# Kernel optimization log

Hardware: AMD Instinct MI355X
Metric: run time of the kernel (lower is better)

The kernel has to match this reference:

```python
import jax, jax.numpy as jnp
import numpy as np

IMAGE_C = 1
IMAGE_W = 28
PIXELS_PER_ROW = IMAGE_W * IMAGE_C  # 28

B, T, E = 16, IMAGE_W * IMAGE_W * IMAGE_C, 512  # T = 784
H = 8
D = E // H  # head_dim = 64


def get_2d_causal_bias(T):
    idx = jnp.arange(T)
    i = idx // PIXELS_PER_ROW          # row index
    j = (idx % PIXELS_PER_ROW) // IMAGE_C  # col index
    c = idx % IMAGE_C                  # channel index
    q_i, k_i = i[:, None], i[None, :]
    q_j, k_j = j[:, None], j[None, :]
    q_c, k_c = c[:, None], c[None, :]
    allowed = (k_i < q_i) | ((k_i == q_i) & (k_j < q_j)) | (
        (k_i == q_i) & (k_j == q_j) & (k_c <= q_c))
    bias = jnp.where(allowed, 0.0, -jnp.inf).astype(jnp.float32)
    return bias[None, None]  # [1, 1, T, T]


def setup_inputs() -> dict:
    key = jax.random.key(0)
    ks = jax.random.split(key, 5)
    s = 1.0 / np.sqrt(E)
    return {
        "x": jax.random.normal(ks[0], (B, T, E), dtype=jnp.float32),
        "Wq": jax.random.normal(ks[1], (E, E), dtype=jnp.float32) * s,
        "bq": jnp.zeros((E,), dtype=jnp.float32),
        "Wk": jax.random.normal(ks[2], (E, E), dtype=jnp.float32) * s,
        "bk": jnp.zeros((E,), dtype=jnp.float32),
        "Wv": jax.random.normal(ks[3], (E, E), dtype=jnp.float32) * s,
        "bv": jnp.zeros((E,), dtype=jnp.float32),
        "Wo": jax.random.normal(ks[4], (E, E), dtype=jnp.float32) * s,
        "bo": jnp.zeros((E,), dtype=jnp.float32),
    }


def reference(x, Wq, bq, Wk, bk, Wv, bv, Wo, bo):
    Bx, Tx, Ex = x.shape
    # projections (torch Linear: y = x @ W.T + b; here W stored as [E, E] used directly)
    Q = (x @ Wq + bq).reshape(Bx, Tx, H, D).transpose(0, 2, 1, 3)  # [B,H,T,D]
    K = (x @ Wk + bk).reshape(Bx, Tx, H, D).transpose(0, 2, 1, 3)
    V = (x @ Wv + bv).reshape(Bx, Tx, H, D).transpose(0, 2, 1, 3)
    scores = jnp.einsum("bhqd,bhkd->bhqk", Q, K) / jnp.sqrt(jnp.float32(D))
    scores = scores + get_2d_causal_bias(Tx)
    attn = jax.nn.softmax(scores, axis=-1)
    ctx = jnp.einsum("bhqk,bhkd->bhqd", attn, V)
    ctx = ctx.transpose(0, 2, 1, 3).reshape(Bx, Tx, Ex)
    return ctx @ Wo + bo
```

## Files before the change

kernel.cpp:

```cpp
#include <hip/hip_runtime.h>
#include <hip/hip_bf16.h>

#define BB    16
#define TT    784
#define TPK   832
#define TPQ   896
#define EE    512
#define HH    8
#define DD    64
#define BT    (BB*TT)

typedef short short8 __attribute__((ext_vector_type(8)));
typedef short short4v __attribute__((ext_vector_type(4)));
typedef float floatx4 __attribute__((ext_vector_type(4)));
typedef float floatx16 __attribute__((ext_vector_type(16)));
typedef unsigned uint4v __attribute__((ext_vector_type(4)));

__device__ __forceinline__ short f2bf(float f) {
    unsigned u = __builtin_bit_cast(unsigned, f);
    u += 0x7FFFu + ((u >> 16) & 1u);
    return (short)(u >> 16);
}

__device__ __forceinline__ unsigned cvtpk_bf16(float lo, float hi) {
    unsigned r;
    asm("v_cvt_pk_bf16_f32 %0, %1, %2" : "=v"(r) : "v"(lo), "v"(hi));
    return r;
}

__device__ __forceinline__ void gload_lds16(const short* g, short* l) {
    __builtin_amdgcn_global_load_lds(
        (const __attribute__((address_space(1))) void*)g,
        (__attribute__((address_space(3))) void*)l, 16, 0, 0);
}

__global__ void prep_kernel(const float* __restrict__ x, short* __restrict__ xb,
                            const float* __restrict__ Wq, const float* __restrict__ Wk,
                            const float* __restrict__ Wv, short* __restrict__ wqkvt,
                            const float* __restrict__ Wo, short* __restrict__ wot,
                            short* __restrict__ Qb, short* __restrict__ Kb, short* __restrict__ Vt)
{
    __shared__ short t[64][65];
    int b = blockIdx.x;
    if (b < 3136) {
        int i = (b * 256 + threadIdx.x) * 8;
        float4 a = *(const float4*)(x + i);
        float4 c = *(const float4*)(x + i + 4);
        short8 o;
        o[0] = f2bf(a.x); o[1] = f2bf(a.y); o[2] = f2bf(a.z); o[3] = f2bf(a.w);
        o[4] = f2bf(c.x); o[5] = f2bf(c.y); o[6] = f2bf(c.z); o[7] = f2bf(c.w);
        *(short8*)(xb + i) = o;
    } else if (b < 3392) {
        const float* W; short* out; int n0, k0;
        if (b < 3328) {
            int tt = b - 3136;
            n0 = (tt % 24) * 64; k0 = (tt / 24) * 64;
            W = (n0 < 512) ? Wq : (n0 < 1024 ? Wk : Wv);
            out = wqkvt;
        } else {
            int tt = b - 3328;
            n0 = (tt % 8) * 64; k0 = (tt / 8) * 64;
            W = Wo; out = wot;
        }
        int nn0 = n0 & 511;
        for (int i = threadIdx.x; i < 4096; i += 256) {
            int r = i >> 6, c = i & 63;
            t[r][c] = f2bf(W[(k0 + r) * 512 + nn0 + c]);
        }
        __syncthreads();
        for (int i = threadIdx.x; i < 4096; i += 256) {
            int nr = i >> 6, kc = i & 63;
            out[(n0 + nr) * 512 + k0 + kc] = t[kc][nr];
        }
    } else {
        int c = (b - 3392) * 256 + threadIdx.x;
        short8 z = (short8){0,0,0,0,0,0,0,0};
        if (c < 114688) {
            int bh = c / 896, j = c - bh * 896;
            *(short8*)&Qb[(bh * TPQ + TT) * 64 + j * 8] = z;
        } else if (c < 163840) {
            int c2 = c - 114688;
            int bh = c2 / 384, j = c2 - bh * 384;
            *(short8*)&Kb[(bh * TPK + TT) * 64 + j * 8] = z;
        } else {
            int c3 = c - 163840;
            int bh = c3 / 384, j = c3 - bh * 384;
            int d = j / 6, m = j - d * 6;
            *(short8*)&Vt[(bh * 64 + d) * TPK + TT + m * 8] = z;
        }
    }
}

__global__ __launch_bounds__(256, 3) void gemm_qkv_kernel(
    const short* __restrict__ A, const short* __restrict__ Bt,
    const float* __restrict__ bq, const float* __restrict__ bk, const float* __restrict__ bv,
    short* __restrict__ Qb, short* __restrict__ Kb, short* __restrict__ Vt)
{
    __shared__ __align__(16) short smem[24576];
    short* As0 = smem;
    short* Bs0 = smem + 12288;

    const int orig = blockIdx.x;
    const int tile = (orig & 7) * 147 + (orig >> 3);
    const int m0 = (tile / 12) * 128, n0 = (tile % 12) * 128;
    const int tid = threadIdx.x;
    const int lane = tid & 63, w = tid >> 6;
    const int wr = w >> 1, wc = w & 1;
    const int l16 = lane & 15, quad = lane >> 4;

    const int sr = tid & 127;
    const int sc = tid >> 7;
    const short* Ag = A  + (size_t)(m0 + sr) * 512 + sc * 8;
    const short* Bg = Bt + (size_t)(n0 + sr) * 512 + sc * 8;

    auto stage = [&](int it) {
        int b = it % 3;
        int ko = it * 32;
        gload_lds16(Ag + ko,      As0 + b * 4096 + tid * 8);
        gload_lds16(Ag + ko + 16, As0 + b * 4096 + 2048 + tid * 8);
        gload_lds16(Bg + ko,      Bs0 + b * 4096 + tid * 8);
        gload_lds16(Bg + ko + 16, Bs0 + b * 4096 + 2048 + tid * 8);
    };

    floatx4 acc[4][4];
    #pragma unroll
    for (int i = 0; i < 4; i++)
        #pragma unroll
        for (int j = 0; j < 4; j++)
            acc[i][j] = (floatx4){0.f, 0.f, 0.f, 0.f};

    stage(0);
    stage(1);

    #pragma unroll
    for (int it = 0; it < 16; it++) {
        if (it < 15) asm volatile("s_waitcnt vmcnt(4)" ::: "memory");
        else         asm volatile("s_waitcnt vmcnt(0)" ::: "memory");
        __builtin_amdgcn_s_barrier();
        __builtin_amdgcn_sched_barrier(0);
        if (it < 14) stage(it + 2);
        const short* as = As0 + (it % 3) * 4096;
        const short* bs = Bs0 + (it % 3) * 4096;
        short8 af[4], bf[4];
        #pragma unroll
        for (int i = 0; i < 4; i++) {
            af[i] = *(const short8*)&as[quad * 1024 + (wr * 64 + i * 16 + l16) * 8];
            bf[i] = *(const short8*)&bs[quad * 1024 + (wc * 64 + i * 16 + l16) * 8];
        }
        #pragma unroll
        for (int mi = 0; mi < 4; mi++)
            #pragma unroll
            for (int ni = 0; ni < 4; ni++)
                acc[mi][ni] = __builtin_amdgcn_mfma_f32_16x16x32_bf16(af[mi], bf[ni], acc[mi][ni], 0, 0, 0);
    }
    __syncthreads();

    const int sel = n0 >> 9;
    if (sel == 2) {
        #pragma unroll
        for (int mi = 0; mi < 4; mi++) {
            int m = m0 + wr * 64 + mi * 16 + quad * 4;
            int bb = m / TT, t = m - bb * TT;
            #pragma unroll
            for (int ni = 0; ni < 4; ni++) {
                int nn = (n0 + wc * 64 + ni * 16 + l16) & 511;
                int hh = nn >> 6, dd = nn & 63;
                float b = bv[nn];
                short4v pv;
                #pragma unroll
                for (int r = 0; r < 4; r++) pv[r] = f2bf(acc[mi][ni][r] + b);
                *(short4v*)&Vt[((size_t)(bb * HH + hh) * 64 + dd) * TPK + t] = pv;
            }
        }
    } else {
        short* Ct = smem;
        const float* bias = (sel == 0) ? bq : bk;
        #pragma unroll
        for (int mi = 0; mi < 4; mi++) {
            #pragma unroll
            for (int ni = 0; ni < 4; ni++) {
                int nl = wc * 64 + ni * 16 + l16;
                int nn = (n0 + nl) & 511;
                float b = bias[nn];
                #pragma unroll
                for (int r = 0; r < 4; r++) {
                    float v = acc[mi][ni][r] + b;
                    if (sel == 0) v *= 0.125f;
                    Ct[(wr * 64 + mi * 16 + quad * 4 + r) * 130 + nl] = f2bf(v);
                }
            }
        }
        __syncthreads();
        short* dst = (sel == 0) ? Qb : Kb;
        const int tp = (sel == 0) ? TPQ : TPK;
        int nl = lane * 2;
        int nn = (n0 + nl) & 511;
        int hh = nn >> 6, dd = nn & 63;
        #pragma unroll 4
        for (int rr = 0; rr < 32; rr++) {
            int ml = w * 32 + rr;
            int m = m0 + ml;
            int bb = m / TT, t = m - bb * TT;
            unsigned pv = *(const unsigned*)&Ct[ml * 130 + nl];
            *(unsigned*)&dst[((bb * HH + hh) * tp + t) * 64 + dd] = pv;
        }
    }
}

__global__ __launch_bounds__(256, 3) void attn_kernel(
    const short* __restrict__ Qb, const short* __restrict__ Kb, const short* __restrict__ Vt,
    short* __restrict__ ctx)
{
    const int g = blockIdx.x;
    const int low = g & 7, rest = g >> 3;
    const int qt = 12 - (rest >> 4);
    const int bh = ((rest & 15) << 3) | low;
    const int bb = bh >> 3, hh = bh & 7;
    const int tid = threadIdx.x;
    const int lane = tid & 63, w = tid >> 6;
    const int wq = w >> 1, wk = w & 1;
    const int l32 = lane & 31, hi = lane >> 5;
    const int r7 = l32 & 7;

    __shared__ __align__(16) short Ks[2][4096];
    __shared__ __align__(16) short Vs[2][4096];

    const short* Kbase = Kb + (size_t)(bh * TPK) * 64;
    const short* Vbase = Vt + (size_t)(bh * 64) * TPK;

    const int srow = tid >> 3;
    const int sc8  = tid & 7;
    const int scol = sc8 * 8;
    const int ksw  = (sc8 ^ (srow & 7)) * 8;
    const int vg0  = (sc8 >> 1) * 2;
    const int vsw0 = ((vg0       ^ (srow & 7)) * 8) + (sc8 & 1) * 4;
    const int vsw1 = (((vg0 + 1) ^ (srow & 7)) * 8) + (sc8 & 1) * 4;

    short8 kreg[2], vreg[2];
    auto load_tile = [&](int kt) {
        #pragma unroll
        for (int p = 0; p < 2; p++) {
            int row = srow + p * 32;
            kreg[p] = *(const short8*)(Kbase + (kt * 64 + row) * 64 + scol);
            vreg[p] = *(const short8*)(Vbase + row * TPK + kt * 64 + scol);
        }
    };
    auto store_tile = [&](int b) {
        #pragma unroll
        for (int p = 0; p < 2; p++) {
            int ro = (srow + p * 32) * 64;
            *(short8*)&Ks[b][ro + ksw] = kreg[p];
            short4v v0, v1;
            #pragma unroll
            for (int i = 0; i < 4; i++) { v0[i] = vreg[p][i]; v1[i] = vreg[p][i + 4]; }
            *(short4v*)&Vs[b][ro + vsw0] = v0;
            *(short4v*)&Vs[b][ro + vsw1] = v1;
        }
    };

    const int q_lo = qt * 64 + wq * 32;
    const int qg = q_lo + l32;
    const bool wreal = (q_lo < TT);
    const short* Qrow = Qb + (size_t)(bh * TPQ + qg) * 64;
    short8 qf[4];
    #pragma unroll
    for (int d = 0; d < 4; d++) qf[d] = *(const short8*)(Qrow + d * 16 + hi * 8);

    floatx16 accO[2];
    #pragma unroll
    for (int dt = 0; dt < 2; dt++)
        #pragma unroll
        for (int i = 0; i < 16; i++) accO[dt][i] = 0.f;
    float accL = 0.f;

    load_tile(0);
    store_tile(0);

    for (int kt = 0; kt <= qt; kt++) {
        const int cb = kt & 1;
        if (kt < qt) load_tile(kt + 1);
        __syncthreads();
        const int kbase = kt * 64 + wk * 32;
        if (wreal && kbase <= q_lo + 31) {
            floatx16 z;
            #pragma unroll
            for (int i = 0; i < 16; i++) z[i] = 0.f;
            #pragma unroll
            for (int d = 0; d < 4; d++) {
                short8 kf = *(const short8*)&Ks[cb][(wk * 32 + l32) * 64 + (((d * 2 + hi) ^ r7) * 8)];
                z = __builtin_amdgcn_mfma_f32_32x32x16_bf16(kf, qf[d], z, 0, 0, 0);
            }
            float p[16];
            #pragma unroll
            for (int r = 0; r < 16; r++) p[r] = __expf(z[r]);
            if (kbase + 31 > q_lo) {
                #pragma unroll
                for (int r = 0; r < 16; r++) {
                    int keyg = kbase + (r & 3) + 8 * (r >> 2) + 4 * hi;
                    if (keyg > qg) p[r] = 0.f;
                }
            }
            #pragma unroll
            for (int r = 0; r < 16; r++) accL += p[r];
            #pragma unroll
            for (int s = 0; s < 2; s++) {
                uint4v pw;
                #pragma unroll
                for (int jj = 0; jj < 4; jj++)
                    pw[jj] = cvtpk_bf16(p[8 * s + 2 * jj], p[8 * s + 2 * jj + 1]);
                short8 pb = __builtin_bit_cast(short8, pw);
                #pragma unroll
                for (int dt = 0; dt < 2; dt++) {
                    short8 vf = *(const short8*)&Vs[cb][(dt * 32 + l32) * 64 + (((wk * 4 + s * 2 + hi) ^ r7) * 8)];
                    accO[dt] = __builtin_amdgcn_mfma_f32_32x32x16_bf16(vf, pb, accO[dt], 0, 0, 0);
                }
            }
        }
        if (kt < qt) store_tile((kt + 1) & 1);
    }

    __syncthreads();
    float* rbuf  = (float*)&Ks[0][0];
    float* rbufL = (float*)&Vs[0][0];
    if (wk == 1) {
        #pragma unroll
        for (int dt = 0; dt < 2; dt++)
            #pragma unroll
            for (int r = 0; r < 16; r++)
                rbuf[((wq * 2 + dt) * 16 + r) * 64 + lane] = accO[dt][r];
        rbufL[wq * 64 + lane] = accL;
    }
    __syncthreads();
    if (wk == 0) {
        #pragma unroll
        for (int dt = 0; dt < 2; dt++)
            #pragma unroll
            for (int r = 0; r < 16; r++)
                accO[dt][r] += rbuf[((wq * 2 + dt) * 16 + r) * 64 + lane];
        accL += rbufL[wq * 64 + lane];
        float Lt = accL + __shfl_xor(accL, 32, 64);
        if (wreal && qg < TT) {
            float inv = 1.f / Lt;
            short* crow = ctx + (size_t)(bb * TT + qg) * 512 + hh * 64;
            #pragma unroll
            for (int dt = 0; dt < 2; dt++)
                #pragma unroll
                for (int g4 = 0; g4 < 4; g4++) {
                    short4v pv;
                    #pragma unroll
                    for (int r4 = 0; r4 < 4; r4++) pv[r4] = f2bf(accO[dt][g4 * 4 + r4] * inv);
                    *(short4v*)&crow[dt * 32 + g4 * 8 + 4 * hi] = pv;
                }
        }
    }
}

__global__ __launch_bounds__(256, 4) void gemm_out_kernel(
    const short* __restrict__ A, const short* __restrict__ Bt,
    const float* __restrict__ bo, float* __restrict__ out)
{
    __shared__ __align__(16) short smem[16384];
    short* As0 = smem;
    short* Bs0 = smem + 8192;

    const int orig = blockIdx.x;
    const int tile = (orig & 7) * 49 + (orig >> 3);
    const int m0 = (tile >> 2) * 128, n0 = (tile & 3) * 128;
    const int tid = threadIdx.x;
    const int lane = tid & 63, w = tid >> 6;
    const int wr = w >> 1, wc = w & 1;
    const int l16 = lane & 15, quad = lane >> 4;

    const int srow = w * 32 + (lane >> 2);
    const int scol = (lane & 3) * 8;
    const short* Ag = A  + (size_t)(m0 + srow) * 512 + scol;
    const short* Bg = Bt + (size_t)(n0 + srow) * 512 + scol;
    short* Abase = As0 + w * 1024;
    short* Bbase = Bs0 + w * 1024;

    auto stage = [&](int it) {
        int b = it & 1;
        int ko = it * 32;
        gload_lds16(Ag + ko,            Abase + b * 4096);
        gload_lds16(Ag + ko + 16 * 512, Abase + b * 4096 + 512);
        gload_lds16(Bg + ko,            Bbase + b * 4096);
        gload_lds16(Bg + ko + 16 * 512, Bbase + b * 4096 + 512);
    };

    floatx4 acc[4][4];
    #pragma unroll
    for (int i = 0; i < 4; i++)
        #pragma unroll
        for (int j = 0; j < 4; j++)
            acc[i][j] = (floatx4){0.f, 0.f, 0.f, 0.f};

    stage(0);
    __syncthreads();

    for (int it = 0; it < 16; it++) {
        if (it < 15) stage(it + 1);
        const short* as = As0 + (it & 1) * 4096;
        const short* bs = Bs0 + (it & 1) * 4096;
        short8 af[4], bf[4];
        #pragma unroll
        for (int i = 0; i < 4; i++) {
            af[i] = *(const short8*)&as[(wr * 64 + i * 16 + l16) * 32 + quad * 8];
            bf[i] = *(const short8*)&bs[(wc * 64 + i * 16 + l16) * 32 + quad * 8];
        }
        #pragma unroll
        for (int mi = 0; mi < 4; mi++)
            #pragma unroll
            for (int ni = 0; ni < 4; ni++)
                acc[mi][ni] = __builtin_amdgcn_mfma_f32_16x16x32_bf16(af[mi], bf[ni], acc[mi][ni], 0, 0, 0);
        __syncthreads();
    }

    #pragma unroll
    for (int mi = 0; mi < 4; mi++) {
        #pragma unroll
        for (int ni = 0; ni < 4; ni++) {
            int n = n0 + wc * 64 + ni * 16 + l16;
            float bias = bo[n];
            #pragma unroll
            for (int r = 0; r < 4; r++) {
                int m = m0 + wr * 64 + mi * 16 + quad * 4 + r;
                out[(size_t)m * 512 + n] = acc[mi][ni][r] + bias;
            }
        }
    }
}

extern "C" void kernel_launch(void* const* d_in, const int* in_sizes, int n_in,
                              void* d_out, int out_size, void* d_ws, size_t ws_size,
                              hipStream_t stream) {
    const float* x  = (const float*)d_in[0];
    const float* Wq = (const float*)d_in[1];
    const float* bq = (const float*)d_in[2];
    const float* Wk = (const float*)d_in[3];
    const float* bk = (const float*)d_in[4];
    const float* Wv = (const float*)d_in[5];
    const float* bv = (const float*)d_in[6];
    const float* Wo = (const float*)d_in[7];
    const float* bo = (const float*)d_in[8];
    float* out = (float*)d_out;

    char* ws = (char*)d_ws;
    size_t off = 0;
    auto alloc = [&](size_t bytes) -> void* {
        void* p = ws + off;
        off += (bytes + 255) & ~(size_t)255;
        return p;
    };
    short* xb    = (short*)alloc((size_t)BT * EE * 2);
    short* wqkvt = (short*)alloc((size_t)1536 * 512 * 2);
    short* wot   = (short*)alloc((size_t)512 * 512 * 2);
    short* Qb    = (short*)alloc((size_t)BB * HH * TPQ * DD * 2);
    short* Kb    = (short*)alloc((size_t)BB * HH * TPK * DD * 2);
    short* Vtb   = (short*)alloc((size_t)BB * HH * DD * TPK * 2);
    short* ctxb  = (short*)alloc((size_t)BT * EE * 2);

    prep_kernel<<<4224, 256, 0, stream>>>(x, xb, Wq, Wk, Wv, wqkvt, Wo, wot, Qb, Kb, Vtb);
    gemm_qkv_kernel<<<1176, 256, 0, stream>>>(xb, wqkvt, bq, bk, bv, Qb, Kb, Vtb);
    attn_kernel<<<1664, 256, 0, stream>>>(Qb, Kb, Vtb, ctxb);
    gemm_out_kernel<<<392, 256, 0, stream>>>(ctxb, wot, bo, out);
}
```

Baseline: 174.4 us.

## Give each attention wave its own query rows; triple-buffer output GEMM

The attention kernel now gives each of the four waves its own 32 query rows over a 128-query block and has each wave process both 32-key halves of a tile. This removes the cross-wave LDS reduction and halves the grid, so each K/V tile staged in LDS is shared by more queries. The output GEMM moves to a three-stage async LDS pipeline with explicit vmcnt waits and a single barrier per iteration, plus a k-major LDS layout. The price is lower occupancy in the GEMM (launch bound 3, more LDS), coarser causal work imbalance, and more serial work per attention wave.

```diff
diff --git a/kernel.cpp b/kernel.cpp
--- a/kernel.cpp
+++ b/kernel.cpp
@@ -213,12 +213,11 @@
 {
     const int g = blockIdx.x;
     const int low = g & 7, rest = g >> 3;
-    const int qt = 12 - (rest >> 4);
+    const int qb = 6 - (rest >> 4);
     const int bh = ((rest & 15) << 3) | low;
     const int bb = bh >> 3, hh = bh & 7;
     const int tid = threadIdx.x;
     const int lane = tid & 63, w = tid >> 6;
-    const int wq = w >> 1, wk = w & 1;
     const int l32 = lane & 31, hi = lane >> 5;
     const int r7 = l32 & 7;
 
@@ -258,9 +257,13 @@
         }
     };
 
-    const int q_lo = qt * 64 + wq * 32;
-    const int qg = q_lo + l32;
+    const int q0   = qb * 128;
+    const int q_lo = q0 + w * 32;
+    const int qg   = q_lo + l32;
     const bool wreal = (q_lo < TT);
+    const int q_top = (q0 + 127 < TT - 1) ? (q0 + 127) : (TT - 1);
+    const int KT = (q_top >> 6) + 1;
+
     const short* Qrow = Qb + (size_t)(bh * TPQ + qg) * 64;
     short8 qf[4];
     #pragma unroll
@@ -276,92 +279,76 @@
     load_tile(0);
     store_tile(0);
 
-    for (int kt = 0; kt <= qt; kt++) {
+    for (int kt = 0; kt < KT; kt++) {
         const int cb = kt & 1;
-        if (kt < qt) load_tile(kt + 1);
+        if (kt < KT - 1) load_tile(kt + 1);
         __syncthreads();
-        const int kbase = kt * 64 + wk * 32;
-        if (wreal && kbase <= q_lo + 31) {
-            floatx16 z;
-            #pragma unroll
-            for (int i = 0; i < 16; i++) z[i] = 0.f;
-            #pragma unroll
-            for (int d = 0; d < 4; d++) {
-                short8 kf = *(const short8*)&Ks[cb][(wk * 32 + l32) * 64 + (((d * 2 + hi) ^ r7) * 8)];
-                z = __builtin_amdgcn_mfma_f32_32x32x16_bf16(kf, qf[d], z, 0, 0, 0);
-            }
-            float p[16];
-            #pragma unroll
-            for (int r = 0; r < 16; r++) p[r] = __expf(z[r]);
-            if (kbase + 31 > q_lo) {
-                #pragma unroll
-                for (int r = 0; r < 16; r++) {
-                    int keyg = kbase + (r & 3) + 8 * (r >> 2) + 4 * hi;
-                    if (keyg > qg) p[r] = 0.f;
+        if (wreal) {
+            #pragma unroll
+            for (int kh = 0; kh < 2; kh++) {
+                const int kbase = kt * 64 + kh * 32;
+                if (kbase > q_lo + 31) continue;
+                floatx16 z;
+                #pragma unroll
+                for (int i = 0; i < 16; i++) z[i] = 0.f;
+                #pragma unroll
+                for (int d = 0; d < 4; d++) {
+                    short8 kf = *(const short8*)&Ks[cb][(kh * 32 + l32) * 64 + (((d * 2 + hi) ^ r7) * 8)];
+                    z = __builtin_amdgcn_mfma_f32_32x32x16_bf16(kf, qf[d], z, 0, 0, 0);
+                }
+                float p[16];
+                #pragma unroll
+                for (int r = 0; r < 16; r++) p[r] = __expf(z[r]);
+                if (kbase + 31 > q_lo) {
+                    #pragma unroll
+                    for (int r = 0; r < 16; r++) {
+                        int keyg = kbase + (r & 3) + 8 * (r >> 2) + 4 * hi;
+                        if (keyg > qg) p[r] = 0.f;
+                    }
+                }
+                #pragma unroll
+                for (int r = 0; r < 16; r++) accL += p[r];
+                #pragma unroll
+                for (int s = 0; s < 2; s++) {
+                    uint4v pw;
+                    #pragma unroll
+                    for (int jj = 0; jj < 4; jj++)
+                        pw[jj] = cvtpk_bf16(p[8 * s + 2 * jj], p[8 * s + 2 * jj + 1]);
+                    short8 pb = __builtin_bit_cast(short8, pw);
+                    #pragma unroll
+                    for (int dt = 0; dt < 2; dt++) {
+                        short8 vf = *(const short8*)&Vs[cb][(dt * 32 + l32) * 64 + (((kh * 4 + s * 2 + hi) ^ r7) * 8)];
+                        accO[dt] = __builtin_amdgcn_mfma_f32_32x32x16_bf16(vf, pb, accO[dt], 0, 0, 0);
+                    }
                 }
             }
-            #pragma unroll
-            for (int r = 0; r < 16; r++) accL += p[r];
-            #pragma unroll
-            for (int s = 0; s < 2; s++) {
-                uint4v pw;
-                #pragma unroll
-                for (int jj = 0; jj < 4; jj++)
-                    pw[jj] = cvtpk_bf16(p[8 * s + 2 * jj], p[8 * s + 2 * jj + 1]);
-                short8 pb = __builtin_bit_cast(short8, pw);
-                #pragma unroll
-                for (int dt = 0; dt < 2; dt++) {
-                    short8 vf = *(const short8*)&Vs[cb][(dt * 32 + l32) * 64 + (((wk * 4 + s * 2 + hi) ^ r7) * 8)];
-                    accO[dt] = __builtin_amdgcn_mfma_f32_32x32x16_bf16(vf, pb, accO[dt], 0, 0, 0);
-                }
+        }
+        if (kt < KT - 1) store_tile((kt + 1) & 1);
+    }
+
+    float Lt = accL + __shfl_xor(accL, 32, 64);
+    if (wreal && qg < TT) {
+        float inv = 1.f / Lt;
+        short* crow = ctx + (size_t)(bb * TT + qg) * 512 + hh * 64;
+        #pragma unroll
+        for (int dt = 0; dt < 2; dt++)
+            #pragma unroll
+            for (int g4 = 0; g4 < 4; g4++) {
+                short4v pv;
+                #pragma unroll
+                for (int r4 = 0; r4 < 4; r4++) pv[r4] = f2bf(accO[dt][g4 * 4 + r4] * inv);
+                *(short4v*)&crow[dt * 32 + g4 * 8 + 4 * hi] = pv;
             }
-        }
-        if (kt < qt) store_tile((kt + 1) & 1);
-    }
-
-    __syncthreads();
-    float* rbuf  = (float*)&Ks[0][0];
-    float* rbufL = (float*)&Vs[0][0];
-    if (wk == 1) {
-        #pragma unroll
-        for (int dt = 0; dt < 2; dt++)
-            #pragma unroll
-            for (int r = 0; r < 16; r++)
-                rbuf[((wq * 2 + dt) * 16 + r) * 64 + lane] = accO[dt][r];
-        rbufL[wq * 64 + lane] = accL;
-    }
-    __syncthreads();
-    if (wk == 0) {
-        #pragma unroll
-        for (int dt = 0; dt < 2; dt++)
-            #pragma unroll
-            for (int r = 0; r < 16; r++)
-                accO[dt][r] += rbuf[((wq * 2 + dt) * 16 + r) * 64 + lane];
-        accL += rbufL[wq * 64 + lane];
-        float Lt = accL + __shfl_xor(accL, 32, 64);
-        if (wreal && qg < TT) {
-            float inv = 1.f / Lt;
-            short* crow = ctx + (size_t)(bb * TT + qg) * 512 + hh * 64;
-            #pragma unroll
-            for (int dt = 0; dt < 2; dt++)
-                #pragma unroll
-                for (int g4 = 0; g4 < 4; g4++) {
-                    short4v pv;
-                    #pragma unroll
-                    for (int r4 = 0; r4 < 4; r4++) pv[r4] = f2bf(accO[dt][g4 * 4 + r4] * inv);
-                    *(short4v*)&crow[dt * 32 + g4 * 8 + 4 * hi] = pv;
-                }
-        }
-    }
-}
-
-__global__ __launch_bounds__(256, 4) void gemm_out_kernel(
+    }
+}
+
+__global__ __launch_bounds__(256, 3) void gemm_out_kernel(
     const short* __restrict__ A, const short* __restrict__ Bt,
     const float* __restrict__ bo, float* __restrict__ out)
 {
-    __shared__ __align__(16) short smem[16384];
+    __shared__ __align__(16) short smem[24576];
     short* As0 = smem;
-    short* Bs0 = smem + 8192;
+    short* Bs0 = smem + 12288;
 
     const int orig = blockIdx.x;
     const int tile = (orig & 7) * 49 + (orig >> 3);
@@ -371,20 +358,18 @@
     const int wr = w >> 1, wc = w & 1;
     const int l16 = lane & 15, quad = lane >> 4;
 
-    const int srow = w * 32 + (lane >> 2);
-    const int scol = (lane & 3) * 8;
-    const short* Ag = A  + (size_t)(m0 + srow) * 512 + scol;
-    const short* Bg = Bt + (size_t)(n0 + srow) * 512 + scol;
-    short* Abase = As0 + w * 1024;
-    short* Bbase = Bs0 + w * 1024;
+    const int sr = tid & 127;
+    const int sc = tid >> 7;
+    const short* Ag = A  + (size_t)(m0 + sr) * 512 + sc * 8;
+    const short* Bg = Bt + (size_t)(n0 + sr) * 512 + sc * 8;
 
     auto stage = [&](int it) {
-        int b = it & 1;
+        int b = it % 3;
         int ko = it * 32;
-        gload_lds16(Ag + ko,            Abase + b * 4096);
-        gload_lds16(Ag + ko + 16 * 512, Abase + b * 4096 + 512);
-        gload_lds16(Bg + ko,            Bbase + b * 4096);
-        gload_lds16(Bg + ko + 16 * 512, Bbase + b * 4096 + 512);
+        gload_lds16(Ag + ko,      As0 + b * 4096 + tid * 8);
+        gload_lds16(Ag + ko + 16, As0 + b * 4096 + 2048 + tid * 8);
+        gload_lds16(Bg + ko,      Bs0 + b * 4096 + tid * 8);
+        gload_lds16(Bg + ko + 16, Bs0 + b * 4096 + 2048 + tid * 8);
     };
 
     floatx4 acc[4][4];
@@ -395,24 +380,28 @@
             acc[i][j] = (floatx4){0.f, 0.f, 0.f, 0.f};
 
     stage(0);
-    __syncthreads();
-
+    stage(1);
+
+    #pragma unroll
     for (int it = 0; it < 16; it++) {
-        if (it < 15) stage(it + 1);
-        const short* as = As0 + (it & 1) * 4096;
-        const short* bs = Bs0 + (it & 1) * 4096;
+        if (it < 15) asm volatile("s_waitcnt vmcnt(4)" ::: "memory");
+        else         asm volatile("s_waitcnt vmcnt(0)" ::: "memory");
+        __builtin_amdgcn_s_barrier();
+        __builtin_amdgcn_sched_barrier(0);
+        if (it < 14) stage(it + 2);
+        const short* as = As0 + (it % 3) * 4096;
+        const short* bs = Bs0 + (it % 3) * 4096;
         short8 af[4], bf[4];
         #pragma unroll
         for (int i = 0; i < 4; i++) {
-            af[i] = *(const short8*)&as[(wr * 64 + i * 16 + l16) * 32 + quad * 8];
-            bf[i] = *(const short8*)&bs[(wc * 64 + i * 16 + l16) * 32 + quad * 8];
+            af[i] = *(const short8*)&as[quad * 1024 + (wr * 64 + i * 16 + l16) * 8];
+            bf[i] = *(const short8*)&bs[quad * 1024 + (wc * 64 + i * 16 + l16) * 8];
         }
         #pragma unroll
         for (int mi = 0; mi < 4; mi++)
             #pragma unroll
             for (int ni = 0; ni < 4; ni++)
                 acc[mi][ni] = __builtin_amdgcn_mfma_f32_16x16x32_bf16(af[mi], bf[ni], acc[mi][ni], 0, 0, 0);
-        __syncthreads();
     }
 
     #pragma unroll
@@ -461,6 +450,6 @@
 
     prep_kernel<<<4224, 256, 0, stream>>>(x, xb, Wq, Wk, Wv, wqkvt, Wo, wot, Qb, Kb, Vtb);
     gemm_qkv_kernel<<<1176, 256, 0, stream>>>(xb, wqkvt, bq, bk, bv, Qb, Kb, Vtb);
-    attn_kernel<<<1664, 256, 0, stream>>>(Qb, Kb, Vtb, ctxb);
+    attn_kernel<<<896, 256, 0, stream>>>(Qb, Kb, Vtb, ctxb);
     gemm_out_kernel<<<392, 256, 0, stream>>>(ctxb, wot, bo, out);
 }
```

Result: slower. 179.8 us (+3.1%).
